# Performance work log

Measured on AMD Instinct MI355X. Metric: run time of the kernel, lower is better.

Reference implementation:

```python
import jax, jax.numpy as jnp
import numpy as np

COMMITMENT_COST = 0.25


def setup_inputs() -> dict:
    key = jax.random.key(0)
    k1, k2 = jax.random.split(key)
    x = jax.random.normal(k1, (32, 1024, 512), dtype=jnp.float32)
    codebook = jax.random.normal(k2, (8192, 512), dtype=jnp.float32)
    return {"x": x, "codebook": codebook}


def reference(x, codebook):
    D = codebook.shape[1]
    flat = x.reshape(-1, D)                                   # [N, D]
    # squared L2 distances: ||f||^2 + ||c||^2 - 2 f c^T
    distances = (
        jnp.sum(flat * flat, axis=1, keepdims=True)
        + jnp.sum(codebook * codebook, axis=1)
        - 2.0 * jnp.matmul(flat, codebook.T)                   # [N, K]
    )
    encoding_indices = jnp.argmin(distances, axis=1)           # [N]
    quantized = codebook[encoding_indices].reshape(x.shape)    # [.., D]
    commitment_loss = COMMITMENT_COST * jnp.mean(
        (jax.lax.stop_gradient(quantized) - x) ** 2
    )
    # straight-through estimator
    quantized_st = x + jax.lax.stop_gradient(quantized - x)
    return (quantized_st, commitment_loss)
```

## Files before the change

kernel.cpp:

```cpp
#include <hip/hip_runtime.h>
#include <stdint.h>

#define N_TOT 32768
#define DDIM  512
#define KCB   8192
#define NSPLIT 4
#define COLS_SPLIT (KCB / NSPLIT)
#define BN 128
#define BC 128
#define BKD 64
#define NTILES (COLS_SPLIT / BC)
#define NSTEPS (NTILES * 8)
#define MARGIN 0.15f

#define RB3 32
#define RP3 32
#define RSLOTS (RGRID3 / RP3)
#define RGRID3 2048

typedef _Float16 half8 __attribute__((ext_vector_type(8)));
typedef float    floatx4 __attribute__((ext_vector_type(4)));

typedef const __attribute__((address_space(1))) unsigned int* gas_ptr;
typedef __attribute__((address_space(3))) unsigned int* las_ptr;
__device__ __forceinline__ void gld_lds16(void* l, const void* g) {
    __builtin_amdgcn_global_load_lds((gas_ptr)g, (las_ptr)l, 16, 0, 0);
}

__device__ __forceinline__ unsigned long long shfl_xor_u64(unsigned long long v, int m) {
    unsigned int lo = (unsigned int)v, hi = (unsigned int)(v >> 32);
    lo = __shfl_xor(lo, m, 64);
    hi = __shfl_xor(hi, m, 64);
    return ((unsigned long long)hi << 32) | lo;
}

__global__ __launch_bounds__(256) void convert_x_kernel(
    const float* __restrict__ x, _Float16* __restrict__ xh) {
    size_t i = ((size_t)blockIdx.x * 256 + threadIdx.x) * 8;
    float4 v0 = *(const float4*)(x + i);
    float4 v1 = *(const float4*)(x + i + 4);
    half8 h;
    h[0] = (_Float16)v0.x; h[1] = (_Float16)v0.y; h[2] = (_Float16)v0.z; h[3] = (_Float16)v0.w;
    h[4] = (_Float16)v1.x; h[5] = (_Float16)v1.y; h[6] = (_Float16)v1.z; h[7] = (_Float16)v1.w;
    *(half8*)(xh + i) = h;
}

__global__ __launch_bounds__(256) void convert_cb_kernel(
    const float* __restrict__ cb, _Float16* __restrict__ cbh, float* __restrict__ cnorm) {
    int row = blockIdx.x * 4 + (threadIdx.x >> 6);
    int lane = threadIdx.x & 63;
    const float* src = cb + (size_t)row * DDIM + lane * 8;
    float4 v0 = *(const float4*)src;
    float4 v1 = *(const float4*)(src + 4);
    half8 h;
    h[0] = (_Float16)v0.x; h[1] = (_Float16)v0.y; h[2] = (_Float16)v0.z; h[3] = (_Float16)v0.w;
    h[4] = (_Float16)v1.x; h[5] = (_Float16)v1.y; h[6] = (_Float16)v1.z; h[7] = (_Float16)v1.w;
    *(half8*)(cbh + (size_t)row * DDIM + lane * 8) = h;
    float s = v0.x*v0.x + v0.y*v0.y + v0.z*v0.z + v0.w*v0.w
            + v1.x*v1.x + v1.y*v1.y + v1.z*v1.z + v1.w*v1.w;
#pragma unroll
    for (int off = 32; off > 0; off >>= 1) s += __shfl_down(s, off, 64);
    if (lane == 0) cnorm[row] = s;
}

__global__ __launch_bounds__(256, 2) void gemm_argmin_kernel(
    const _Float16* __restrict__ xh, const _Float16* __restrict__ cbh,
    const float* __restrict__ cnorm,
    float* __restrict__ sb1, int* __restrict__ si1, float* __restrict__ sb2) {

    __shared__ __align__(16) _Float16 smem[32768];

    const int tid = threadIdx.x;
    const int wave = tid >> 6;
    const int lane = tid & 63;
    const int rowHalf = wave >> 1;
    const int colHalf = wave & 1;
    const int l15 = lane & 15;
    const int quad = lane >> 4;

    const int orig = blockIdx.x;
    const int wg = ((orig & 7) << 7) | (orig >> 3);
    const int bx = wg & 255;
    const int by = wg >> 8;
    const int row0 = bx * BN;
    const int colBase = by * COLS_SPLIT;

    float b1[16], b2[16];
    int   i1[16];
#pragma unroll
    for (int s = 0; s < 16; ++s) { b1[s] = 3.402823466e38f; b2[s] = 3.402823466e38f; i1[s] = 0; }

#define STAGE(par, tilev, d0v) do {                                             \
        _Float16* Asb = smem + (par) * 16384;                                   \
        _Float16* Bsb = Asb + 8192;                                             \
        const int col0s = colBase + (tilev) * BC;                               \
        _Pragma("unroll")                                                       \
        for (int r = 0; r < 4; ++r) {                                           \
            int c = wave * 256 + r * 64 + lane;                                 \
            int ar = c >> 3;                                                    \
            int q  = (c & 7) ^ (ar & 7);        \
            gld_lds16(Asb + (wave * 256 + r * 64) * 8,                          \
                      xh + (((size_t)(row0 + ar)) << 9) + (d0v) + q * 8);       \
            gld_lds16(Bsb + (wave * 256 + r * 64) * 8,                          \
                      cbh + (((size_t)(col0s + ar)) << 9) + (d0v) + q * 8);     \
        }                                                                       \
    } while (0)

    floatx4 acc[4][4];
#pragma unroll
    for (int i = 0; i < 4; ++i)
#pragma unroll
        for (int j = 0; j < 4; ++j)
            acc[i][j] = (floatx4){0.f, 0.f, 0.f, 0.f};

    STAGE(0, 0, 0);
    __syncthreads();

    for (int s = 0; s < NSTEPS; ++s) {
        const int par = s & 1;
        if (s + 1 < NSTEPS) {
            STAGE((s + 1) & 1, (s + 1) >> 3, ((s + 1) & 7) * BKD);
        }
        _Float16* As = smem + par * 16384;
        _Float16* Bs = As + 8192;
#pragma unroll
        for (int kh = 0; kh < 2; ++kh) {
            half8 af[4], bf[4];
#pragma unroll
            for (int i = 0; i < 4; ++i) {
                int rr = rowHalf * 64 + i * 16 + l15;
                int qs = (kh * 4 + quad) ^ (rr & 7);
                af[i] = *(const half8*)(As + rr * 64 + qs * 8);
            }
#pragma unroll
            for (int j = 0; j < 4; ++j) {
                int cc = colHalf * 64 + j * 16 + l15;
                int qs = (kh * 4 + quad) ^ (cc & 7);
                bf[j] = *(const half8*)(Bs + cc * 64 + qs * 8);
            }
#pragma unroll
            for (int i = 0; i < 4; ++i)
#pragma unroll
                for (int j = 0; j < 4; ++j)
                    acc[i][j] = __builtin_amdgcn_mfma_f32_16x16x32_f16(
                        af[i], bf[j], acc[i][j], 0, 0, 0);
        }
        if ((s & 7) == 7) {
            const int col0 = colBase + (s >> 3) * BC;
#pragma unroll
            for (int j = 0; j < 4; ++j) {
                int col = col0 + colHalf * 64 + j * 16 + l15;
                float cn = cnorm[col];
#pragma unroll
                for (int i = 0; i < 4; ++i) {
#pragma unroll
                    for (int r = 0; r < 4; ++r) {
                        float sc = fmaf(-2.0f, acc[i][j][r], cn);
                        int slot = i * 4 + r;
                        if (sc < b1[slot]) { b2[slot] = b1[slot]; b1[slot] = sc; i1[slot] = col; }
                        else if (sc < b2[slot]) b2[slot] = sc;
                    }
                }
            }
#pragma unroll
            for (int i = 0; i < 4; ++i)
#pragma unroll
                for (int j = 0; j < 4; ++j)
                    acc[i][j] = (floatx4){0.f, 0.f, 0.f, 0.f};
        }
        __syncthreads();
    }
#undef STAGE

#pragma unroll
    for (int m = 1; m < 16; m <<= 1) {
#pragma unroll
        for (int s = 0; s < 16; ++s) {
            float ob1 = __shfl_xor(b1[s], m, 64);
            float ob2 = __shfl_xor(b2[s], m, 64);
            int   oi1 = __shfl_xor(i1[s], m, 64);
            if (ob1 < b1[s] || (ob1 == b1[s] && oi1 < i1[s])) {
                b2[s] = fminf(b1[s], ob2);
                b1[s] = ob1; i1[s] = oi1;
            } else {
                b2[s] = fminf(b2[s], ob1);
            }
        }
    }

    float* mb1 = (float*)smem;
    float* mb2 = mb1 + 256;
    int*   mi1 = (int*)(mb2 + 256);
    if (l15 == 0) {
#pragma unroll
        for (int s = 0; s < 16; ++s) {
            int row = rowHalf * 64 + (s >> 2) * 16 + quad * 4 + (s & 3);
            mb1[colHalf * 128 + row] = b1[s];
            mb2[colHalf * 128 + row] = b2[s];
            mi1[colHalf * 128 + row] = i1[s];
        }
    }
    __syncthreads();
    if (tid < 128) {
        float a1 = mb1[tid], a2 = mb2[tid]; int ai = mi1[tid];
        float c1 = mb1[128 + tid], c2 = mb2[128 + tid]; int ci = mi1[128 + tid];
        float r1, r2; int ri;
        if (c1 < a1 || (c1 == a1 && ci < ai)) { r1 = c1; ri = ci; r2 = fminf(a1, c2); }
        else { r1 = a1; ri = ai; r2 = fminf(a2, c1); }
        size_t o = (size_t)by * N_TOT + row0 + tid;
        sb1[o] = r1; si1[o] = ri; sb2[o] = r2;
    }
}

__global__ __launch_bounds__(256) void merge_kernel(
    const float* __restrict__ sb1, const int* __restrict__ si1, const float* __restrict__ sb2,
    int* __restrict__ indices, int* __restrict__ flags,
    int* __restrict__ list, int* __restrict__ count,
    unsigned long long* __restrict__ result) {
    int n = blockIdx.x * 256 + threadIdx.x;
    float b1 = sb1[n]; int i1 = si1[n]; float b2 = sb2[n];
#pragma unroll
    for (int s = 1; s < NSPLIT; ++s) {
        float ob1 = sb1[(size_t)s * N_TOT + n];
        int   oi1 = si1[(size_t)s * N_TOT + n];
        float ob2 = sb2[(size_t)s * N_TOT + n];
        if (ob1 < b1 || (ob1 == b1 && oi1 < i1)) { b2 = fminf(b1, ob2); b1 = ob1; i1 = oi1; }
        else b2 = fminf(b2, ob1);
    }
    indices[n] = i1;
    result[n] = 0xFFFFFFFFFFFFFFFFull;
    int f = (b2 - b1 < MARGIN) ? 1 : 0;
    flags[n] = f;
    if (f) { int pos = atomicAdd(count, 1); list[pos] = n; }
}

__global__ __launch_bounds__(256) void repair3_kernel(
    const float* __restrict__ x, const float* __restrict__ cb,
    const float* __restrict__ cnorm, const int* __restrict__ list,
    const int* __restrict__ count, unsigned long long* __restrict__ result) {
    __shared__ __align__(16) float xs[RB3][512];
    __shared__ unsigned long long red[RB3][4];
    const int tid = threadIdx.x;
    const int lane = tid & 63;
    const int wv = tid >> 6;
    const int part = blockIdx.x & (RP3 - 1);
    const int slot0 = blockIdx.x >> 5;
    const int cnt = *count;
    const int nbatch = (cnt + RB3 - 1) / RB3;
    const int k = part * 256 + tid;
    const float cn = cnorm[k];
    const float* crow = cb + (size_t)k * 512;

    for (int batch = slot0; batch < nbatch; batch += RSLOTS) {
        const int rb = min(RB3, cnt - batch * RB3);
        __syncthreads();
        for (int t = tid; t < rb * 128; t += 256) {
            int b = t >> 7, d4 = t & 127;
            int n = list[batch * RB3 + b];
            ((float4*)xs[b])[d4] = ((const float4*)(x + ((size_t)n << 9)))[d4];
        }
        __syncthreads();

        float d0[RB3], d1[RB3], d2[RB3], d3[RB3];
#pragma unroll
        for (int b = 0; b < RB3; ++b) { d0[b] = 0.f; d1[b] = 0.f; d2[b] = 0.f; d3[b] = 0.f; }

        for (int t = 0; t < 512; t += 16) {
            float4 c0 = *(const float4*)(crow + t);
            float4 c1 = *(const float4*)(crow + t + 4);
            float4 c2 = *(const float4*)(crow + t + 8);
            float4 c3 = *(const float4*)(crow + t + 12);
#pragma unroll
            for (int b = 0; b < RB3; ++b) {
                float4 x0 = *(const float4*)&xs[b][t];
                float4 x1 = *(const float4*)&xs[b][t + 4];
                float4 x2 = *(const float4*)&xs[b][t + 8];
                float4 x3 = *(const float4*)&xs[b][t + 12];
                d0[b] = fmaf(c0.x, x0.x, d0[b]);  d0[b] = fmaf(c0.y, x0.y, d0[b]);
                d0[b] = fmaf(c0.z, x0.z, d0[b]);  d0[b] = fmaf(c0.w, x0.w, d0[b]);
                d1[b] = fmaf(c1.x, x1.x, d1[b]);  d1[b] = fmaf(c1.y, x1.y, d1[b]);
                d1[b] = fmaf(c1.z, x1.z, d1[b]);  d1[b] = fmaf(c1.w, x1.w, d1[b]);
                d2[b] = fmaf(c2.x, x2.x, d2[b]);  d2[b] = fmaf(c2.y, x2.y, d2[b]);
                d2[b] = fmaf(c2.z, x2.z, d2[b]);  d2[b] = fmaf(c2.w, x2.w, d2[b]);
                d3[b] = fmaf(c3.x, x3.x, d3[b]);  d3[b] = fmaf(c3.y, x3.y, d3[b]);
                d3[b] = fmaf(c3.z, x3.z, d3[b]);  d3[b] = fmaf(c3.w, x3.w, d3[b]);
            }
        }

#pragma unroll
        for (int b = 0; b < RB3; ++b) {
            float s = cn - 2.f * ((d0[b] + d1[b]) + (d2[b] + d3[b]));
            unsigned int sb = __float_as_uint(s);
            sb = (sb & 0x80000000u) ? ~sb : (sb | 0x80000000u);
            unsigned long long p = ((unsigned long long)sb << 32) | (unsigned int)k;
#pragma unroll
            for (int m = 32; m > 0; m >>= 1) {
                unsigned long long o = shfl_xor_u64(p, m);
                if (o < p) p = o;
            }
            if (lane == 0) red[b][wv] = p;
        }
        __syncthreads();
        if (tid < RB3) {
            unsigned long long p = red[tid][0];
            if (red[tid][1] < p) p = red[tid][1];
            if (red[tid][2] < p) p = red[tid][2];
            if (red[tid][3] < p) p = red[tid][3];
            if (tid < rb) {
                int n = list[batch * RB3 + tid];
                atomicMin(&result[n], p);
            }
        }
    }
}

__global__ __launch_bounds__(256) void fixup_kernel(
    const int* __restrict__ flags, const unsigned long long* __restrict__ result,
    int* __restrict__ indices) {
    int n = blockIdx.x * 256 + threadIdx.x;
    if (flags[n]) indices[n] = (int)(result[n] & 0xFFFFFFFFu);
}

__global__ void cnorm_kernel(const float* __restrict__ cb, float* __restrict__ cnorm) {
    int wave = (blockIdx.x * blockDim.x + threadIdx.x) >> 6;
    int lane = threadIdx.x & 63;
    if (wave >= KCB) return;
    const float* row = cb + (size_t)wave * DDIM;
    float s = 0.f;
#pragma unroll
    for (int j = 0; j < DDIM / 64; ++j) { float v = row[lane + 64 * j]; s += v * v; }
#pragma unroll
    for (int off = 32; off > 0; off >>= 1) s += __shfl_down(s, off, 64);
    if (lane == 0) cnorm[wave] = s;
}

#define FBN 64
#define FBD 32
#define FLDA (FBN + 4)
__global__ __launch_bounds__(256) void argmin_fp32_kernel(
    const float* __restrict__ x, const float* __restrict__ cb,
    const float* __restrict__ cnorm, int* __restrict__ indices) {
    __shared__ float As[FBD][FLDA];
    __shared__ float Bs[FBD][FLDA];
    __shared__ float redv[FBN][16];
    __shared__ int   redi[FBN][16];
    const int tid = threadIdx.x;
    const int tx = tid & 15, ty = tid >> 4;
    const int row0 = blockIdx.x * FBN;
    float best[4]; int bidx[4];
#pragma unroll
    for (int i = 0; i < 4; ++i) { best[i] = 3.402823466e+38f; bidx[i] = KCB; }
    for (int k0 = 0; k0 < KCB; k0 += 64) {
        float acc[4][4] = {};
        for (int d0 = 0; d0 < DDIM; d0 += FBD) {
#pragma unroll
            for (int t = 0; t < 2; ++t) {
                int q = tid + t * 256, rr = q >> 3, dq = q & 7;
                float4 v = *(const float4*)(x + (size_t)(row0 + rr) * DDIM + d0 + dq * 4);
                As[dq*4+0][rr] = v.x; As[dq*4+1][rr] = v.y; As[dq*4+2][rr] = v.z; As[dq*4+3][rr] = v.w;
                float4 w = *(const float4*)(cb + (size_t)(k0 + rr) * DDIM + d0 + dq * 4);
                Bs[dq*4+0][rr] = w.x; Bs[dq*4+1][rr] = w.y; Bs[dq*4+2][rr] = w.z; Bs[dq*4+3][rr] = w.w;
            }
            __syncthreads();
#pragma unroll
            for (int d = 0; d < FBD; ++d) {
                float4 av = *(const float4*)&As[d][ty * 4];
                float4 bv = *(const float4*)&Bs[d][tx * 4];
                float a[4] = {av.x, av.y, av.z, av.w}, b[4] = {bv.x, bv.y, bv.z, bv.w};
#pragma unroll
                for (int i = 0; i < 4; ++i)
#pragma unroll
                    for (int j = 0; j < 4; ++j) acc[i][j] += a[i] * b[j];
            }
            __syncthreads();
        }
#pragma unroll
        for (int j = 0; j < 4; ++j) {
            int k = k0 + tx * 4 + j;
            float cn = cnorm[k];
#pragma unroll
            for (int i = 0; i < 4; ++i) {
                float s = cn - 2.0f * acc[i][j];
                if (s < best[i] || (s == best[i] && k < bidx[i])) { best[i] = s; bidx[i] = k; }
            }
        }
    }
#pragma unroll
    for (int i = 0; i < 4; ++i) { redv[ty*4+i][tx] = best[i]; redi[ty*4+i][tx] = bidx[i]; }
    __syncthreads();
    if (tid < FBN) {
        float bv = redv[tid][0]; int bi = redi[tid][0];
#pragma unroll
        for (int t = 1; t < 16; ++t) {
            float v = redv[tid][t]; int ii = redi[tid][t];
            if (v < bv || (v == bv && ii < bi)) { bv = v; bi = ii; }
        }
        indices[row0 + tid] = bi;
    }
}

__global__ __launch_bounds__(256) void output_kernel(
    const float* __restrict__ x, const float* __restrict__ cb,
    const int* __restrict__ indices, float* __restrict__ out,
    float* __restrict__ loss_acc) {
    size_t base = ((size_t)blockIdx.x * blockDim.x + threadIdx.x) * 16;
    int n = (int)(base >> 9);
    int d = (int)(base & 511);
    int idx = indices[n];
    const float* cr = cb + (size_t)idx * DDIM + d;
    const float* xr = x + base;
    float* orow = out + base;
    float lsum = 0.f;
#pragma unroll
    for (int t = 0; t < 4; ++t) {
        float4 q  = *(const float4*)(cr + t * 4);
        float4 xv = *(const float4*)(xr + t * 4);
        float dx0 = q.x - xv.x, dx1 = q.y - xv.y, dx2 = q.z - xv.z, dx3 = q.w - xv.w;
        float4 o;
        o.x = xv.x + dx0; o.y = xv.y + dx1; o.z = xv.z + dx2; o.w = xv.w + dx3;
        *(float4*)(orow + t * 4) = o;
        lsum += dx0*dx0 + dx1*dx1 + dx2*dx2 + dx3*dx3;
    }
#pragma unroll
    for (int off = 32; off > 0; off >>= 1) lsum += __shfl_down(lsum, off, 64);
    __shared__ float wsum[4];
    int lane = threadIdx.x & 63, wv = threadIdx.x >> 6;
    if (lane == 0) wsum[wv] = lsum;
    __syncthreads();
    if (threadIdx.x == 0) atomicAdd(loss_acc, wsum[0] + wsum[1] + wsum[2] + wsum[3]);
}

__global__ void finalize_kernel(const float* __restrict__ loss_acc, float* __restrict__ out_loss) {
    *out_loss = (*loss_acc) * (0.25f / (float)((size_t)N_TOT * DDIM));
}

extern "C" void kernel_launch(void* const* d_in, const int* in_sizes, int n_in,
                              void* d_out, int out_size, void* d_ws, size_t ws_size,
                              hipStream_t stream) {
    const float* x  = (const float*)d_in[0];
    const float* cb = (const float*)d_in[1];
    float* out = (float*)d_out;

    char* ws = (char*)d_ws;
    float* loss_acc = (float*)ws;
    int*   count    = (int*)(ws + 8);
    int*   indices  = (int*)(ws + 256);
    int*   flags    = (int*)(ws + 256 + 131072);
    float* cnorm    = (float*)(ws + 256 + 2 * 131072);
    int*   list     = (int*)(ws + 256 + 2 * 131072 + 32768);
    unsigned long long* result =
        (unsigned long long*)(ws + 256 + 3 * 131072 + 32768);
    size_t off = 256 + 3 * 131072 + 32768 + 262144;
    _Float16* xh  = (_Float16*)(ws + off);
    _Float16* cbh = (_Float16*)(ws + off + (size_t)N_TOT * DDIM * 2);
    size_t soff = off + (size_t)N_TOT * DDIM * 2 + (size_t)KCB * DDIM * 2;
    float* sb1 = (float*)(ws + soff);
    int*   si1 = (int*)(ws + soff + (size_t)NSPLIT * N_TOT * 4);
    float* sb2 = (float*)(ws + soff + (size_t)NSPLIT * N_TOT * 8);
    size_t need = soff + (size_t)NSPLIT * N_TOT * 12;

    hipMemsetAsync(ws, 0, 16, stream);
    if (ws_size >= need) {
        convert_x_kernel<<<(N_TOT * DDIM) / (256 * 8), 256, 0, stream>>>(x, xh);
        convert_cb_kernel<<<KCB / 4, 256, 0, stream>>>(cb, cbh, cnorm);
        gemm_argmin_kernel<<<(N_TOT / BN) * NSPLIT, 256, 0, stream>>>(
            xh, cbh, cnorm, sb1, si1, sb2);
        merge_kernel<<<N_TOT / 256, 256, 0, stream>>>(sb1, si1, sb2, indices, flags,
                                                      list, count, result);
        repair3_kernel<<<RGRID3, 256, 0, stream>>>(x, cb, cnorm, list, count, result);
        fixup_kernel<<<N_TOT / 256, 256, 0, stream>>>(flags, result, indices);
    } else {
        cnorm_kernel<<<KCB / 4, 256, 0, stream>>>(cb, cnorm);
        argmin_fp32_kernel<<<N_TOT / FBN, 256, 0, stream>>>(x, cb, cnorm, indices);
    }
    output_kernel<<<((size_t)N_TOT * DDIM) / (256 * 16), 256, 0, stream>>>(
        x, cb, indices, out, loss_acc);
    finalize_kernel<<<1, 1, 0, stream>>>(loss_acc, out + (size_t)N_TOT * DDIM);
}
```

Before: 834.3 us.

## Triple-buffer GEMM-argmin with BKD=32, one barrier per step, and higher occupancy

The fp16 distance GEMM's K-chunk drops from 64 to 32 and the LDS ring grows from two buffers to three, so two loads are in flight ahead of compute. The per-step __syncthreads is replaced by a partial vmcnt wait plus a raw barrier. Launch bounds rise to 3 blocks per CU thanks to the smaller LDS footprint, and MFMA sections get a raised wave priority. Precomputed load and LDS offsets with a new swizzle cut address arithmetic, at the cost of more loop iterations and barriers plus tighter register budgets.

```diff
diff --git a/kernel.cpp b/kernel.cpp
--- a/kernel.cpp
+++ b/kernel.cpp
@@ -8,9 +8,9 @@
 #define COLS_SPLIT (KCB / NSPLIT)
 #define BN 128
 #define BC 128
-#define BKD 64
+#define BKD 32
 #define NTILES (COLS_SPLIT / BC)
-#define NSTEPS (NTILES * 8)
+#define NSTEPS (NTILES * 16)
 #define MARGIN 0.15f
 
 #define RB3 32
@@ -63,12 +63,13 @@
     if (lane == 0) cnorm[row] = s;
 }
 
-__global__ __launch_bounds__(256, 2) void gemm_argmin_kernel(
+__global__ __launch_bounds__(256, 3) void gemm_argmin_kernel(
     const _Float16* __restrict__ xh, const _Float16* __restrict__ cbh,
     const float* __restrict__ cnorm,
     float* __restrict__ sb1, int* __restrict__ si1, float* __restrict__ sb2) {
 
-    __shared__ __align__(16) _Float16 smem[32768];
+    __shared__ __align__(16) _Float16 smem[24576];
+    char* smemb = (char*)smem;
 
     const int tid = threadIdx.x;
     const int wave = tid >> 6;
@@ -85,27 +86,86 @@
     const int row0 = bx * BN;
     const int colBase = by * COLS_SPLIT;
 
+    int voff2[2];
+#pragma unroll
+    for (int r = 0; r < 2; ++r) {
+        int c = wave * 128 + r * 64 + lane;
+        int ar = c >> 2;
+        int g  = (c & 3) ^ ((ar >> 1) & 3);
+        voff2[r] = (ar << 9) + g * 8;
+    }
+    const _Float16* aptr = xh + ((size_t)row0 << 9);
+    const _Float16* bptr = cbh + ((size_t)colBase << 9);
+
+    int aoffs[4], boffs[4];
+#pragma unroll
+    for (int i = 0; i < 4; ++i) {
+        int rr = rowHalf * 64 + i * 16 + l15;
+        aoffs[i] = rr * 64 + (quad ^ ((rr >> 1) & 3)) * 16;
+        int cc = colHalf * 64 + i * 16 + l15;
+        boffs[i] = 8192 + cc * 64 + (quad ^ ((cc >> 1) & 3)) * 16;
+    }
+
     float b1[16], b2[16];
     int   i1[16];
 #pragma unroll
     for (int s = 0; s < 16; ++s) { b1[s] = 3.402823466e38f; b2[s] = 3.402823466e38f; i1[s] = 0; }
 
-#define STAGE(par, tilev, d0v) do {                                             \
-        _Float16* Asb = smem + (par) * 16384;                                   \
-        _Float16* Bsb = Asb + 8192;                                             \
-        const int col0s = colBase + (tilev) * BC;                               \
+#define STAGE(bi, st) do {                                                      \
+        _Float16* Asb = smem + (bi) * 8192;                                     \
+        _Float16* Bsb = Asb + 4096;                                             \
+        const int boffu = ((st) >> 4) << 16;          \
+        const int d0v   = ((st) & 15) * BKD;                                    \
         _Pragma("unroll")                                                       \
-        for (int r = 0; r < 4; ++r) {                                           \
-            int c = wave * 256 + r * 64 + lane;                                 \
-            int ar = c >> 3;                                                    \
-            int q  = (c & 7) ^ (ar & 7);        \
-            gld_lds16(Asb + (wave * 256 + r * 64) * 8,                          \
-                      xh + (((size_t)(row0 + ar)) << 9) + (d0v) + q * 8);       \
-            gld_lds16(Bsb + (wave * 256 + r * 64) * 8,                          \
-                      cbh + (((size_t)(col0s + ar)) << 9) + (d0v) + q * 8);     \
+        for (int r = 0; r < 2; ++r) {                                           \
+            gld_lds16(Asb + (wave * 128 + r * 64) * 8,                          \
+                      aptr + d0v + voff2[r]);                                   \
+            gld_lds16(Bsb + (wave * 128 + r * 64) * 8,                          \
+                      bptr + boffu + d0v + voff2[r]);                           \
         }                                                                       \
     } while (0)
 
+#define COMPUTE(sv) do {                                                        \
+        const char* Ab = smemb + bufr * 16384;                                  \
+        half8 af[4], bf[4];                                                     \
+        _Pragma("unroll")                                                       \
+        for (int i = 0; i < 4; ++i) af[i] = *(const half8*)(Ab + aoffs[i]);     \
+        _Pragma("unroll")                                                       \
+        for (int j = 0; j < 4; ++j) bf[j] = *(const half8*)(Ab + boffs[j]);     \
+        __builtin_amdgcn_s_setprio(1);                                          \
+        _Pragma("unroll")                                                       \
+        for (int i = 0; i < 4; ++i)                                             \
+            _Pragma("unroll")                                                   \
+            for (int j = 0; j < 4; ++j)                                         \
+                acc[i][j] = __builtin_amdgcn_mfma_f32_16x16x32_f16(             \
+                    af[i], bf[j], acc[i][j], 0, 0, 0);                          \
+        __builtin_amdgcn_s_setprio(0);                                          \
+        if (((sv) & 15) == 15) {                                                \
+            const int col0 = colBase + ((sv) >> 4) * BC;                        \
+            _Pragma("unroll")                                                   \
+            for (int j = 0; j < 4; ++j) {                                       \
+                int col = col0 + colHalf * 64 + j * 16 + l15;                   \
+                float cn = cnorm[col];                                          \
+                _Pragma("unroll")                                               \
+                for (int i = 0; i < 4; ++i) {                                   \
+                    _Pragma("unroll")                                           \
+                    for (int r = 0; r < 4; ++r) {                               \
+                        float sc = fmaf(-2.0f, acc[i][j][r], cn);               \
+                        int slot = i * 4 + r;                                   \
+                        if (sc < b1[slot]) { b2[slot] = b1[slot]; b1[slot] = sc; i1[slot] = col; } \
+                        else if (sc < b2[slot]) b2[slot] = sc;                  \
+                    }                                                           \
+                }                                                               \
+            }                                                                   \
+            _Pragma("unroll")                                                   \
+            for (int i = 0; i < 4; ++i)                                         \
+                _Pragma("unroll")                                               \
+                for (int j = 0; j < 4; ++j)                                     \
+                    acc[i][j] = (floatx4){0.f, 0.f, 0.f, 0.f};                  \
+        }                                                                       \
+        bufr = (bufr == 2) ? 0 : bufr + 1;                                      \
+    } while (0)
+
     floatx4 acc[4][4];
 #pragma unroll
     for (int i = 0; i < 4; ++i)
@@ -113,64 +173,29 @@
         for (int j = 0; j < 4; ++j)
             acc[i][j] = (floatx4){0.f, 0.f, 0.f, 0.f};
 
-    STAGE(0, 0, 0);
+    STAGE(0, 0);
+    STAGE(1, 1);
+    int bufr = 0;
+    int bufw = 2;
+
+    for (int s = 0; s < NSTEPS - 1; ++s) {
+        asm volatile("s_waitcnt vmcnt(4)" ::: "memory");
+        __builtin_amdgcn_s_barrier();
+        __builtin_amdgcn_sched_barrier(0);
+        if (s < NSTEPS - 2) {
+            STAGE(bufw, s + 2);
+            bufw = (bufw == 2) ? 0 : bufw + 1;
+        }
+        COMPUTE(s);
+    }
+    asm volatile("s_waitcnt vmcnt(0)" ::: "memory");
+    __builtin_amdgcn_s_barrier();
+    __builtin_amdgcn_sched_barrier(0);
+    COMPUTE(NSTEPS - 1);
+#undef STAGE
+#undef COMPUTE
+
     __syncthreads();
-
-    for (int s = 0; s < NSTEPS; ++s) {
-        const int par = s & 1;
-        if (s + 1 < NSTEPS) {
-            STAGE((s + 1) & 1, (s + 1) >> 3, ((s + 1) & 7) * BKD);
-        }
-        _Float16* As = smem + par * 16384;
-        _Float16* Bs = As + 8192;
-#pragma unroll
-        for (int kh = 0; kh < 2; ++kh) {
-            half8 af[4], bf[4];
-#pragma unroll
-            for (int i = 0; i < 4; ++i) {
-                int rr = rowHalf * 64 + i * 16 + l15;
-                int qs = (kh * 4 + quad) ^ (rr & 7);
-                af[i] = *(const half8*)(As + rr * 64 + qs * 8);
-            }
-#pragma unroll
-            for (int j = 0; j < 4; ++j) {
-                int cc = colHalf * 64 + j * 16 + l15;
-                int qs = (kh * 4 + quad) ^ (cc & 7);
-                bf[j] = *(const half8*)(Bs + cc * 64 + qs * 8);
-            }
-#pragma unroll
-            for (int i = 0; i < 4; ++i)
-#pragma unroll
-                for (int j = 0; j < 4; ++j)
-                    acc[i][j] = __builtin_amdgcn_mfma_f32_16x16x32_f16(
-                        af[i], bf[j], acc[i][j], 0, 0, 0);
-        }
-        if ((s & 7) == 7) {
-            const int col0 = colBase + (s >> 3) * BC;
-#pragma unroll
-            for (int j = 0; j < 4; ++j) {
-                int col = col0 + colHalf * 64 + j * 16 + l15;
-                float cn = cnorm[col];
-#pragma unroll
-                for (int i = 0; i < 4; ++i) {
-#pragma unroll
-                    for (int r = 0; r < 4; ++r) {
-                        float sc = fmaf(-2.0f, acc[i][j][r], cn);
-                        int slot = i * 4 + r;
-                        if (sc < b1[slot]) { b2[slot] = b1[slot]; b1[slot] = sc; i1[slot] = col; }
-                        else if (sc < b2[slot]) b2[slot] = sc;
-                    }
-                }
-            }
-#pragma unroll
-            for (int i = 0; i < 4; ++i)
-#pragma unroll
-                for (int j = 0; j < 4; ++j)
-                    acc[i][j] = (floatx4){0.f, 0.f, 0.f, 0.f};
-        }
-        __syncthreads();
-    }
-#undef STAGE
 
 #pragma unroll
     for (int m = 1; m < 16; m <<= 1) {
```

Result: slower. 930.7 us (+11.6%).
